# Kernel optimization log

Measured on AMD Instinct MI355X. Metric: run time of the kernel, lower is better.

The kernel has to match this reference:

```python
import jax, jax.numpy as jnp
import numpy as np

E = 8          # moe_num_experts
F = 4096       # ffn_hidden_size
D = 2048       # d_model
TOP_K = 2


def setup_inputs() -> dict:
    key = jax.random.key(0)
    k_x, k_r, k_w1, k_v1, k_w2 = jax.random.split(key, 5)
    scale = 0.02  # ~ normal initializer scale
    x = jax.random.normal(k_x, (2, 2048, D), dtype=jnp.float32)
    router_w = jax.random.normal(k_r, (D, E), dtype=jnp.float32) * scale
    w1 = jax.random.normal(k_w1, (E * F, D), dtype=jnp.float32) * scale
    v1 = jax.random.normal(k_v1, (E * F, D), dtype=jnp.float32) * scale
    w2 = jax.random.normal(k_w2, (E * F, D), dtype=jnp.float32) * scale
    return {"x": x, "router_w": router_w, "w1": w1, "v1": v1, "w2": w2}


def reference(x, router_w, w1, v1, w2):
    # --- Router: dense logits -> softmax (fp32) -> top-k -> L1 normalize ---
    logits = jnp.einsum("bsd,de->bse", x.astype(jnp.float32), router_w)
    weights = jax.nn.softmax(logits, axis=-1)                       # [B,S,E]
    top_weights, top_experts = jax.lax.top_k(weights, TOP_K)        # [B,S,K]
    # moe_normalize_expert_weights = 1 -> L1 norm
    top_weights = top_weights / jnp.sum(jnp.abs(top_weights), axis=-1, keepdims=True)
    top_weights = top_weights.astype(x.dtype)

    # --- Experts: dense per-expert GLU, masked combine (faithful to source) ---
    w1r = w1.reshape(E, F, D)
    v1r = v1.reshape(E, F, D)
    w2r = w2.reshape(E, F, D)
    out = jnp.zeros_like(x)
    for e in range(E):  # fixed small structural loop over experts
        x1 = jnp.einsum("bsd,fd->bsf", x, w1r[e])
        x2 = jnp.einsum("bsd,fd->bsf", x, v1r[e])
        h = jax.nn.silu(x1) * x2                                    # GLU
        y = jnp.einsum("bsf,fd->bsd", h, w2r[e])
        coef = jnp.sum((top_experts == e) * top_weights, axis=-1)[:, :, None]
        out = out + coef * y
    return out
```

## Files before the change

### kernel.cpp

```cpp
#include <hip/hip_runtime.h>
#include <cstdio>
#include <cstdint>

typedef _Float16 f16;
typedef _Float16 f16x8 __attribute__((ext_vector_type(8)));
typedef float f32x4 __attribute__((ext_vector_type(4)));

#define D_MODEL 2048
#define FFN     4096
#define FFN2    8192
#define NEXP    8
#define NTOK    4096
#define NENT    (NTOK*2)
#define BM      256
#define BN      256
#define BK      64
#define MAX_ROWS  10240
#define MAX_TILES 40

__device__ __forceinline__ void gload_lds16(const void* g, void* l) {
  __builtin_amdgcn_global_load_lds(
      (const __attribute__((address_space(1))) void*)g,
      (__attribute__((address_space(3))) void*)l, 16, 0, 0);
}

template<int N> __device__ __forceinline__ void waitvm() {
  if constexpr (N == 0) asm volatile("s_waitcnt vmcnt(0)" ::: "memory");
  else if constexpr (N == 2) asm volatile("s_waitcnt vmcnt(2)" ::: "memory");
  else if constexpr (N == 4) asm volatile("s_waitcnt vmcnt(4)" ::: "memory");
  else if constexpr (N == 6) asm volatile("s_waitcnt vmcnt(6)" ::: "memory");
}

template<int LD>
__device__ __forceinline__ void stageA(const f16* aT, int k0, f16* AS, int mh, int tid) {
#pragma unroll
  for (int s = 0; s < 2; s++) {
    int o = s*8192 + tid*16;
    int rl = o >> 7;
    int ce = ((o & 127) ^ ((rl & 7) << 4)) >> 1;
    int arow = s*128 + mh*64 + (rl & 63);
    gload_lds16(aT + (size_t)arow * LD + k0 + ce,
                (char*)AS + mh*16384 + s*8192 + (tid & ~63)*16);
  }
}

template<int LD>
__device__ __forceinline__ void stageB(const f16* bT, int k0, f16* BS, int nh, int tid) {
#pragma unroll
  for (int s = 0; s < 2; s++) {
    int o = s*8192 + tid*16;
    int rl = o >> 7;
    int ce = ((o & 127) ^ ((rl & 7) << 4)) >> 1;
    int crow = (rl >> 5)*64 + nh*32 + (rl & 31);
    gload_lds16(bT + (size_t)crow * LD + k0 + ce,
                (char*)BS + nh*16384 + s*8192 + (tid & ~63)*16);
  }
}

__device__ __forceinline__ f16x8 fragLd(const f16* S, int row, int lane, int ks) {
  int kb = ks*64 + (lane >> 4)*16;
  int off = (row*128 + kb) ^ ((row & 7) << 4);
  return *(const f16x8*)((const char*)S + off);
}

template<int LD, int V0, int V1, int V3, bool SB0, bool SB1, bool SA1, bool SA0>
__device__ __forceinline__ void tile4(
    const f16* aT, const f16* bT, int k1, int k2,
    f16* ASc, f16* BSc, f16* ASn, f16* BSn,
    f32x4 (&acc)[8][4], f16x8 (&aF)[4][2], f16x8 (&bF)[2][2][2],
    int tid, int lane, int wrM, int wcN) {
#pragma unroll
  for (int mf = 0; mf < 4; mf++)
#pragma unroll
    for (int ks = 0; ks < 2; ks++)
      aF[mf][ks] = fragLd(ASc, wrM*64 + mf*16 + (lane & 15), lane, ks);
#pragma unroll
  for (int nf = 0; nf < 2; nf++)
#pragma unroll
    for (int ks = 0; ks < 2; ks++)
      bF[0][nf][ks] = fragLd(BSc, wcN*32 + nf*16 + (lane & 15), lane, ks);
  if constexpr (SB0) stageB<LD>(bT, k1, BSn, 0, tid);
  __builtin_amdgcn_s_barrier();
  __builtin_amdgcn_s_setprio(1);
#pragma unroll
  for (int mf = 0; mf < 4; mf++)
#pragma unroll
    for (int nf = 0; nf < 2; nf++)
#pragma unroll
      for (int ks = 0; ks < 2; ks++)
        acc[mf][nf] = __builtin_amdgcn_mfma_f32_16x16x32_f16(aF[mf][ks], bF[0][nf][ks], acc[mf][nf], 0, 0, 0);
  __builtin_amdgcn_s_setprio(0);
  waitvm<V0>();
  __builtin_amdgcn_s_barrier();
#pragma unroll
  for (int nf = 0; nf < 2; nf++)
#pragma unroll
    for (int ks = 0; ks < 2; ks++)
      bF[1][nf][ks] = fragLd(BSc, 128 + wcN*32 + nf*16 + (lane & 15), lane, ks);
  if constexpr (SB1) stageB<LD>(bT, k1, BSn, 1, tid);
  __builtin_amdgcn_s_barrier();
  __builtin_amdgcn_s_setprio(1);
#pragma unroll
  for (int mf = 0; mf < 4; mf++)
#pragma unroll
    for (int nf = 0; nf < 2; nf++)
#pragma unroll
      for (int ks = 0; ks < 2; ks++)
        acc[mf][2+nf] = __builtin_amdgcn_mfma_f32_16x16x32_f16(aF[mf][ks], bF[1][nf][ks], acc[mf][2+nf], 0, 0, 0);
  __builtin_amdgcn_s_setprio(0);
  waitvm<V1>();
  __builtin_amdgcn_s_barrier();
#pragma unroll
  for (int mf = 0; mf < 4; mf++)
#pragma unroll
    for (int ks = 0; ks < 2; ks++)
      aF[mf][ks] = fragLd(ASc, 128 + wrM*64 + mf*16 + (lane & 15), lane, ks);
  if constexpr (SA1) stageA<LD>(aT, k1, ASn, 1, tid);
  __builtin_amdgcn_s_barrier();
  __builtin_amdgcn_s_setprio(1);
#pragma unroll
  for (int mf = 0; mf < 4; mf++)
#pragma unroll
    for (int nf = 0; nf < 2; nf++)
#pragma unroll
      for (int ks = 0; ks < 2; ks++)
        acc[4+mf][nf] = __builtin_amdgcn_mfma_f32_16x16x32_f16(aF[mf][ks], bF[0][nf][ks], acc[4+mf][nf], 0, 0, 0);
  __builtin_amdgcn_s_setprio(0);
  __builtin_amdgcn_s_barrier();
  if constexpr (SA0) stageA<LD>(aT, k2, ASc, 0, tid);
  __builtin_amdgcn_s_barrier();
  __builtin_amdgcn_s_setprio(1);
#pragma unroll
  for (int mf = 0; mf < 4; mf++)
#pragma unroll
    for (int nf = 0; nf < 2; nf++)
#pragma unroll
      for (int ks = 0; ks < 2; ks++)
        acc[4+mf][2+nf] = __builtin_amdgcn_mfma_f32_16x16x32_f16(aF[mf][ks], bF[1][nf][ks], acc[4+mf][2+nf], 0, 0, 0);
  __builtin_amdgcn_s_setprio(0);
  waitvm<V3>();
  __builtin_amdgcn_s_barrier();
}


__global__ void zero_counts_kernel(int* counts) {
  if (threadIdx.x < NEXP) counts[threadIdx.x] = 0;
}

__global__ void zero_f32_kernel(float* p, int n4) {
  int i = blockIdx.x * blockDim.x + threadIdx.x;
  int stride = gridDim.x * blockDim.x;
  float4 z = {0.f, 0.f, 0.f, 0.f};
  for (; i < n4; i += stride) ((float4*)p)[i] = z;
}

__global__ __launch_bounds__(64) void router_kernel(
    const float* __restrict__ x, const float* __restrict__ rw,
    int* counts, int* te, float* tw, int* trank) {
  int t = blockIdx.x;
  int lane = threadIdx.x;
  float acc[8] = {0.f,0.f,0.f,0.f,0.f,0.f,0.f,0.f};
  const float* xr = x + (size_t)t * D_MODEL;
  for (int d = lane; d < D_MODEL; d += 64) {
    float xv = xr[d];
    const float4* r4 = (const float4*)(rw + (size_t)d * NEXP);
    float4 a = r4[0], b = r4[1];
    acc[0] += xv*a.x; acc[1] += xv*a.y; acc[2] += xv*a.z; acc[3] += xv*a.w;
    acc[4] += xv*b.x; acc[5] += xv*b.y; acc[6] += xv*b.z; acc[7] += xv*b.w;
  }
#pragma unroll
  for (int off = 32; off > 0; off >>= 1) {
#pragma unroll
    for (int e = 0; e < 8; e++) acc[e] += __shfl_down(acc[e], off);
  }
  if (lane == 0) {
    int e0 = 0;
#pragma unroll
    for (int e = 1; e < 8; e++) if (acc[e] > acc[e0]) e0 = e;
    int e1 = (e0 == 0) ? 1 : 0;
#pragma unroll
    for (int e = 0; e < 8; e++) if (e != e0 && acc[e] > acc[e1]) e1 = e;
    float c0 = 1.0f / (1.0f + expf(acc[e1] - acc[e0]));
    float c1 = 1.0f - c0;
    int r0 = atomicAdd(&counts[e0], 1);
    int r1 = atomicAdd(&counts[e1], 1);
    te[t*2] = e0; te[t*2+1] = e1;
    tw[t*2] = c0; tw[t*2+1] = c1;
    trank[t*2] = r0; trank[t*2+1] = r1;
  }
}

__global__ void sched_kernel(const int* counts, int* offsets, int4* sched, int* nT) {
  if (threadIdx.x != 0 || blockIdx.x != 0) return;
  int off = 0, n = 0;
  for (int e = 0; e < NEXP; e++) {
    offsets[e] = off;
    int cnt = counts[e];
    int nt = (cnt + BM - 1) / BM;
    for (int i = 0; i < nt; i++) {
      sched[n] = make_int4(e, off + i*BM, min(BM, cnt - i*BM), 0);
      n++;
    }
    off += nt * BM;
  }
  offsets[NEXP] = off;
  *nT = n;
}

__global__ __launch_bounds__(256) void gather_kernel(
    const float* __restrict__ x, const int* __restrict__ te,
    const float* __restrict__ tw, const int* __restrict__ trank,
    const int* __restrict__ offsets, f16* __restrict__ xg,
    int* __restrict__ token_of, float* __restrict__ coefs) {
  int i = blockIdx.x;
  int t = i >> 1;
  int e = te[i];
  int slot = offsets[e] + trank[i];
  if (threadIdx.x == 0) { token_of[slot] = t; coefs[slot] = tw[i]; }
  const float4* src = (const float4*)(x + (size_t)t * D_MODEL);
  f16x8* dst = (f16x8*)(xg + (size_t)slot * D_MODEL);
  for (int j = threadIdx.x; j < D_MODEL/8; j += 256) {
    float4 v0 = src[j*2], v1 = src[j*2+1];
    f16x8 h;
    h[0]=(f16)v0.x; h[1]=(f16)v0.y; h[2]=(f16)v0.z; h[3]=(f16)v0.w;
    h[4]=(f16)v1.x; h[5]=(f16)v1.y; h[6]=(f16)v1.z; h[7]=(f16)v1.w;
    dst[j] = h;
  }
}

__global__ __launch_bounds__(256) void convert_ileave_kernel(
    const float* __restrict__ src, f16* __restrict__ dst, int parity) {
  int n8 = NEXP*FFN*D_MODEL/8;
  int stride = gridDim.x * 256;
  for (int i = blockIdx.x*256 + threadIdx.x; i < n8; i += stride) {
    int d8 = i & (D_MODEL/8 - 1);
    int fr_glob = i >> 8;
    int e = fr_glob >> 12;
    int fr = fr_glob & (FFN - 1);
    int cr = ((fr >> 4)*2 + parity)*16 + (fr & 15);
    float4 v0 = ((const float4*)src)[(size_t)i*2];
    float4 v1 = ((const float4*)src)[(size_t)i*2 + 1];
    f16x8 h;
    h[0]=(f16)v0.x; h[1]=(f16)v0.y; h[2]=(f16)v0.z; h[3]=(f16)v0.w;
    h[4]=(f16)v1.x; h[5]=(f16)v1.y; h[6]=(f16)v1.z; h[7]=(f16)v1.w;
    ((f16x8*)dst)[((size_t)e*FFN2 + cr)*(D_MODEL/8) + d8] = h;
  }
}

__global__ __launch_bounds__(256) void transpose_w2_kernel(
    const float* __restrict__ w2, f16* __restrict__ w2t) {
  __shared__ float tl[64][65];
  int e = blockIdx.z;
  int d0 = blockIdx.x * 64, f0 = blockIdx.y * 64;
  const float* src = w2 + (size_t)e * FFN * D_MODEL;
  int tid = threadIdx.x;
  int fr = tid >> 4, c4 = (tid & 15) * 4;
#pragma unroll
  for (int rr = 0; rr < 4; rr++) {
    float4 v = *(const float4*)(src + (size_t)(f0 + fr + rr*16) * D_MODEL + d0 + c4);
    tl[fr + rr*16][c4+0] = v.x; tl[fr + rr*16][c4+1] = v.y;
    tl[fr + rr*16][c4+2] = v.z; tl[fr + rr*16][c4+3] = v.w;
  }
  __syncthreads();
  int dr = tid >> 2, fg = (tid & 3) * 16;
  f16* dst = w2t + (size_t)e * D_MODEL * FFN + (size_t)(d0 + dr) * FFN + f0 + fg;
  f16 tmp[16];
#pragma unroll
  for (int j = 0; j < 16; j++) tmp[j] = (f16)tl[fg + j][dr];
  *(float4*)(dst)     = *(float4*)(tmp);
  *(float4*)(dst + 8) = *(float4*)(tmp + 8);
}

__global__ __launch_bounds__(512, 2) void phaseA_kernel(
    const f16* __restrict__ xg, const f16* __restrict__ w12h,
    f16* __restrict__ hbuf, const int4* __restrict__ sched, const int* __restrict__ nT) {
  int tile = blockIdx.y;
  if (tile >= *nT) return;
  int4 sc = sched[tile];
  int e = sc.x, row0 = sc.y;
  int fc0 = blockIdx.x * BN;

  __shared__ f16 AS[2][BM*BK];
  __shared__ f16 BS[2][BN*BK];

  int tid = threadIdx.x, lane = tid & 63, wid = tid >> 6;
  int wrM = wid >> 2, wcN = wid & 3;

  const f16* aT = xg  + (size_t)row0 * D_MODEL;
  const f16* bT = w12h + (size_t)e * FFN2 * D_MODEL + (size_t)fc0 * D_MODEL;

  f32x4 acc[8][4]; f16x8 aF[4][2]; f16x8 bF[2][2][2];
  f32x4 z4 = {0.f,0.f,0.f,0.f};
#pragma unroll
  for (int m = 0; m < 8; m++)
#pragma unroll
    for (int n = 0; n < 4; n++) acc[m][n] = z4;

  stageA<D_MODEL>(aT, 0, AS[0], 0, tid);
  stageB<D_MODEL>(bT, 0, BS[0], 0, tid);
  stageB<D_MODEL>(bT, 0, BS[0], 1, tid);
  stageA<D_MODEL>(aT, 0, AS[0], 1, tid);
  stageA<D_MODEL>(aT, BK, AS[1], 0, tid);
  waitvm<6>();
  __builtin_amdgcn_s_barrier();

  constexpr int NTILES = D_MODEL / BK;
  for (int t = 0; t + 2 < NTILES; t++) {
    int b = t & 1;
    tile4<D_MODEL,6,6,6,true,true,true,true>(aT, bT, (t+1)*BK, (t+2)*BK,
        AS[b], BS[b], AS[b^1], BS[b^1], acc, aF, bF, tid, lane, wrM, wcN);
  }
  { int b = (NTILES-2) & 1;
    tile4<D_MODEL,6,6,4,true,true,true,false>(aT, bT, (NTILES-1)*BK, 0,
        AS[b], BS[b], AS[b^1], BS[b^1], acc, aF, bF, tid, lane, wrM, wcN); }
  { int b = (NTILES-1) & 1;
    tile4<D_MODEL,2,0,-1,false,false,false,false>(aT, bT, 0, 0,
        AS[b], BS[b], AS[b^1], BS[b^1], acc, aF, bF, tid, lane, wrM, wcN); }

  int i15 = lane & 15, l4 = lane >> 4;
#pragma unroll
  for (int m = 0; m < 8; m++) {
    int rowl = wrM*128 + (m>>2)*64 + (m&3)*16 + l4*4;
#pragma unroll
    for (int nh = 0; nh < 2; nh++) {
      int f = (fc0 >> 1) + wcN*32 + nh*16 + i15;
      f16* hb = hbuf + (size_t)(row0 + rowl) * FFN + f;
#pragma unroll
      for (int q = 0; q < 4; q++) {
        float x1 = acc[m][nh*2+0][q], x2 = acc[m][nh*2+1][q];
        float hv = x1 / (1.0f + __expf(-x1)) * x2;
        hb[(size_t)q * FFN] = (f16)hv;
      }
    }
  }
}

__global__ __launch_bounds__(512, 2) void phaseB_kernel(
    const f16* __restrict__ hbuf, const f16* __restrict__ w2t,
    float* __restrict__ out, const int4* __restrict__ sched, const int* __restrict__ nT,
    const int* __restrict__ token_of, const float* __restrict__ coefs) {
  int tile = blockIdx.y;
  if (tile >= *nT) return;
  int4 sc = sched[tile];
  int e = sc.x, row0 = sc.y, valid = sc.z;
  int dc0 = blockIdx.x * BN;

  __shared__ f16 AS[2][BM*BK];
  __shared__ f16 BS[2][BN*BK];

  int tid = threadIdx.x, lane = tid & 63, wid = tid >> 6;
  int wrM = wid >> 2, wcN = wid & 3;

  const f16* aT = hbuf + (size_t)row0 * FFN;
  const f16* bT = w2t + (size_t)e * D_MODEL * FFN + (size_t)dc0 * FFN;

  f32x4 acc[8][4]; f16x8 aF[4][2]; f16x8 bF[2][2][2];
  f32x4 z4 = {0.f,0.f,0.f,0.f};
#pragma unroll
  for (int m = 0; m < 8; m++)
#pragma unroll
    for (int n = 0; n < 4; n++) acc[m][n] = z4;

  stageA<FFN>(aT, 0, AS[0], 0, tid);
  stageB<FFN>(bT, 0, BS[0], 0, tid);
  stageB<FFN>(bT, 0, BS[0], 1, tid);
  stageA<FFN>(aT, 0, AS[0], 1, tid);
  stageA<FFN>(aT, BK, AS[1], 0, tid);
  waitvm<6>();
  __builtin_amdgcn_s_barrier();

  constexpr int NTILES = FFN / BK;
  for (int t = 0; t + 2 < NTILES; t++) {
    int b = t & 1;
    tile4<FFN,6,6,6,true,true,true,true>(aT, bT, (t+1)*BK, (t+2)*BK,
        AS[b], BS[b], AS[b^1], BS[b^1], acc, aF, bF, tid, lane, wrM, wcN);
  }
  { int b = (NTILES-2) & 1;
    tile4<FFN,6,6,4,true,true,true,false>(aT, bT, (NTILES-1)*BK, 0,
        AS[b], BS[b], AS[b^1], BS[b^1], acc, aF, bF, tid, lane, wrM, wcN); }
  { int b = (NTILES-1) & 1;
    tile4<FFN,2,0,-1,false,false,false,false>(aT, bT, 0, 0,
        AS[b], BS[b], AS[b^1], BS[b^1], acc, aF, bF, tid, lane, wrM, wcN); }

  int i15 = lane & 15, l4 = lane >> 4;
#pragma unroll
  for (int m = 0; m < 8; m++) {
#pragma unroll
    for (int q = 0; q < 4; q++) {
      int rl = wrM*128 + (m>>2)*64 + (m&3)*16 + l4*4 + q;
      if (rl < valid) {
        int slot = row0 + rl;
        int t = token_of[slot];
        float cf = coefs[slot];
        float* orow = out + (size_t)t * D_MODEL + dc0 + wcN*64;
#pragma unroll
        for (int n = 0; n < 4; n++)
          atomicAdd(orow + (n>>1)*32 + (n&1)*16 + i15, cf * acc[m][n][q]);
      }
    }
  }
}

extern "C" void kernel_launch(void* const* d_in, const int* in_sizes, int n_in,
                              void* d_out, int out_size, void* d_ws, size_t ws_size,
                              hipStream_t stream) {
  const float* x  = (const float*)d_in[0];
  const float* rw = (const float*)d_in[1];
  const float* w1 = (const float*)d_in[2];
  const float* v1 = (const float*)d_in[3];
  const float* w2 = (const float*)d_in[4];
  float* out = (float*)d_out;

  char* p = (char*)d_ws;
  auto alloc = [&](size_t bytes) {
    char* r = p;
    p += (bytes + 255) & ~(size_t)255;
    return r;
  };
  int*   counts   = (int*)  alloc(NEXP * 4);
  int*   nT       = (int*)  alloc(4);
  int*   offsets  = (int*)  alloc((NEXP + 1) * 4);
  int*   te       = (int*)  alloc(NENT * 4);
  float* tw       = (float*)alloc(NENT * 4);
  int*   trank    = (int*)  alloc(NENT * 4);
  int*   token_of = (int*)  alloc(MAX_ROWS * 4);
  float* coefs    = (float*)alloc(MAX_ROWS * 4);
  int4*  sched    = (int4*) alloc(MAX_TILES * 16);
  f16*   xg       = (f16*)  alloc((size_t)MAX_ROWS * D_MODEL * 2);
  f16*   hbuf     = (f16*)  alloc((size_t)MAX_ROWS * FFN * 2);
  f16*   w12h     = (f16*)  alloc((size_t)NEXP * FFN2 * D_MODEL * 2);
  f16*   w2t      = (f16*)  alloc((size_t)NEXP * FFN * D_MODEL * 2);
  size_t needed = (size_t)(p - (char*)d_ws);
  if (needed > ws_size) {
    fprintf(stderr, "kernel_launch: ws too small: need %zu, have %zu\n", needed, ws_size);
    return;
  }

  zero_counts_kernel<<<1, 64, 0, stream>>>(counts);
  zero_f32_kernel<<<2048, 256, 0, stream>>>(out, out_size / 4);
  router_kernel<<<NTOK, 64, 0, stream>>>(x, rw, counts, te, tw, trank);
  sched_kernel<<<1, 1, 0, stream>>>(counts, offsets, sched, nT);
  gather_kernel<<<NENT, 256, 0, stream>>>(x, te, tw, trank, offsets, xg, token_of, coefs);
  convert_ileave_kernel<<<4096, 256, 0, stream>>>(w1, w12h, 0);
  convert_ileave_kernel<<<4096, 256, 0, stream>>>(v1, w12h, 1);
  transpose_w2_kernel<<<dim3(D_MODEL/64, FFN/64, NEXP), 256, 0, stream>>>(w2, w2t);
  phaseA_kernel<<<dim3(FFN2/BN, MAX_TILES), 512, 0, stream>>>(xg, w12h, hbuf, sched, nT);
  phaseB_kernel<<<dim3(D_MODEL/BN, MAX_TILES), 512, 0, stream>>>(hbuf, w2t, out, sched, nT, token_of, coefs);
}
```

Measured before the change: 945.0 us.

## Split-K the down-projection GEMM and replace atomics with a gather combine kernel

The second expert GEMM is split four ways along the FFN dimension, which raises the block count so more CUs are busy. Each split writes fp16 partial results into reused workspace buffers (xg and w12h) instead of doing fp32 atomicAdd scatter into the output. A new combine kernel gathers each token's two expert slots across all splits, applies the routing weights and writes the output once, so the separate output-zeroing kernel is removed. The cost is extra partial-result traffic, fp16 rounding of the partial sums, and reliance on the reused buffers being large enough and no longer needed.

After: 897.8 us. 1.05x faster.

```diff
diff --git a/kernel.cpp b/kernel.cpp
--- a/kernel.cpp
+++ b/kernel.cpp
@@ -15,6 +15,8 @@
 #define BM      256
 #define BN      256
 #define BK      64
+#define KSPLIT  4
+#define KCHUNK  (FFN / KSPLIT)
 #define MAX_ROWS  10240
 #define MAX_TILES 40
 
@@ -145,13 +147,6 @@
 
 __global__ void zero_counts_kernel(int* counts) {
   if (threadIdx.x < NEXP) counts[threadIdx.x] = 0;
-}
-
-__global__ void zero_f32_kernel(float* p, int n4) {
-  int i = blockIdx.x * blockDim.x + threadIdx.x;
-  int stride = gridDim.x * blockDim.x;
-  float4 z = {0.f, 0.f, 0.f, 0.f};
-  for (; i < n4; i += stride) ((float4*)p)[i] = z;
 }
 
 __global__ __launch_bounds__(64) void router_kernel(
@@ -337,13 +332,14 @@
 
 __global__ __launch_bounds__(512, 2) void phaseB_kernel(
     const f16* __restrict__ hbuf, const f16* __restrict__ w2t,
-    float* __restrict__ out, const int4* __restrict__ sched, const int* __restrict__ nT,
-    const int* __restrict__ token_of, const float* __restrict__ coefs) {
+    f16* __restrict__ yb0, f16* __restrict__ ybR,
+    const int4* __restrict__ sched, const int* __restrict__ nT) {
   int tile = blockIdx.y;
   if (tile >= *nT) return;
   int4 sc = sched[tile];
-  int e = sc.x, row0 = sc.y, valid = sc.z;
+  int e = sc.x, row0 = sc.y;
   int dc0 = blockIdx.x * BN;
+  int z = blockIdx.z;
 
   __shared__ f16 AS[2][BM*BK];
   __shared__ f16 BS[2][BN*BK];
@@ -351,8 +347,8 @@
   int tid = threadIdx.x, lane = tid & 63, wid = tid >> 6;
   int wrM = wid >> 2, wcN = wid & 3;
 
-  const f16* aT = hbuf + (size_t)row0 * FFN;
-  const f16* bT = w2t + (size_t)e * D_MODEL * FFN + (size_t)dc0 * FFN;
+  const f16* aT = hbuf + (size_t)row0 * FFN + z * KCHUNK;
+  const f16* bT = w2t + (size_t)e * D_MODEL * FFN + (size_t)dc0 * FFN + z * KCHUNK;
 
   f32x4 acc[8][4]; f16x8 aF[4][2]; f16x8 bF[2][2][2];
   f32x4 z4 = {0.f,0.f,0.f,0.f};
@@ -369,7 +365,7 @@
   waitvm<6>();
   __builtin_amdgcn_s_barrier();
 
-  constexpr int NTILES = FFN / BK;
+  constexpr int NTILES = KCHUNK / BK;
   for (int t = 0; t + 2 < NTILES; t++) {
     int b = t & 1;
     tile4<FFN,6,6,6,true,true,true,true>(aT, bT, (t+1)*BK, (t+2)*BK,
@@ -382,23 +378,45 @@
     tile4<FFN,2,0,-1,false,false,false,false>(aT, bT, 0, 0,
         AS[b], BS[b], AS[b^1], BS[b^1], acc, aF, bF, tid, lane, wrM, wcN); }
 
+  f16* yb = (z == 0) ? yb0 : (ybR + (size_t)(z-1) * MAX_ROWS * D_MODEL);
   int i15 = lane & 15, l4 = lane >> 4;
 #pragma unroll
   for (int m = 0; m < 8; m++) {
 #pragma unroll
     for (int q = 0; q < 4; q++) {
       int rl = wrM*128 + (m>>2)*64 + (m&3)*16 + l4*4 + q;
-      if (rl < valid) {
-        int slot = row0 + rl;
-        int t = token_of[slot];
-        float cf = coefs[slot];
-        float* orow = out + (size_t)t * D_MODEL + dc0 + wcN*64;
-#pragma unroll
-        for (int n = 0; n < 4; n++)
-          atomicAdd(orow + (n>>1)*32 + (n&1)*16 + i15, cf * acc[m][n][q]);
-      }
+      f16* yrow = yb + (size_t)(row0 + rl) * D_MODEL + dc0 + wcN*64;
+#pragma unroll
+      for (int n = 0; n < 4; n++)
+        yrow[(n>>1)*32 + (n&1)*16 + i15] = (f16)acc[m][n][q];
     }
   }
+}
+
+__global__ __launch_bounds__(256) void combine_kernel(
+    const f16* __restrict__ yb0, const f16* __restrict__ ybR,
+    const int* __restrict__ te, const float* __restrict__ tw,
+    const int* __restrict__ trank, const int* __restrict__ offsets,
+    float* __restrict__ out) {
+  int t = blockIdx.x;
+  int d8 = threadIdx.x;
+  int s0 = offsets[te[2*t]]   + trank[2*t];
+  int s1 = offsets[te[2*t+1]] + trank[2*t+1];
+  float w0 = tw[2*t], w1 = tw[2*t+1];
+  float sum[8] = {0.f,0.f,0.f,0.f,0.f,0.f,0.f,0.f};
+#pragma unroll
+  for (int z = 0; z < KSPLIT; z++) {
+    const f16* yb = (z == 0) ? yb0 : (ybR + (size_t)(z-1) * MAX_ROWS * D_MODEL);
+    f16x8 a = ((const f16x8*)(yb + (size_t)s0 * D_MODEL))[d8];
+    f16x8 b = ((const f16x8*)(yb + (size_t)s1 * D_MODEL))[d8];
+#pragma unroll
+    for (int j = 0; j < 8; j++) sum[j] += w0 * (float)a[j] + w1 * (float)b[j];
+  }
+  float* o = out + (size_t)t * D_MODEL + d8*8;
+  float4 o0 = {sum[0], sum[1], sum[2], sum[3]};
+  float4 o1 = {sum[4], sum[5], sum[6], sum[7]};
+  ((float4*)o)[0] = o0;
+  ((float4*)o)[1] = o1;
 }
 
 extern "C" void kernel_launch(void* const* d_in, const int* in_sizes, int n_in,
@@ -435,9 +453,10 @@
     fprintf(stderr, "kernel_launch: ws too small: need %zu, have %zu\n", needed, ws_size);
     return;
   }
+  f16* yb0 = xg;
+  f16* ybR = w12h;
 
   zero_counts_kernel<<<1, 64, 0, stream>>>(counts);
-  zero_f32_kernel<<<2048, 256, 0, stream>>>(out, out_size / 4);
   router_kernel<<<NTOK, 64, 0, stream>>>(x, rw, counts, te, tw, trank);
   sched_kernel<<<1, 1, 0, stream>>>(counts, offsets, sched, nT);
   gather_kernel<<<NENT, 256, 0, stream>>>(x, te, tw, trank, offsets, xg, token_of, coefs);
@@ -445,5 +464,6 @@
   convert_ileave_kernel<<<4096, 256, 0, stream>>>(v1, w12h, 1);
   transpose_w2_kernel<<<dim3(D_MODEL/64, FFN/64, NEXP), 256, 0, stream>>>(w2, w2t);
   phaseA_kernel<<<dim3(FFN2/BN, MAX_TILES), 512, 0, stream>>>(xg, w12h, hbuf, sched, nT);
-  phaseB_kernel<<<dim3(D_MODEL/BN, MAX_TILES), 512, 0, stream>>>(hbuf, w2t, out, sched, nT, token_of, coefs);
-}
+  phaseB_kernel<<<dim3(D_MODEL/BN, MAX_TILES, KSPLIT), 512, 0, stream>>>(hbuf, w2t, yb0, ybR, sched, nT);
+  combine_kernel<<<NTOK, 256, 0, stream>>>(yb0, ybR, te, tw, trank, offsets, out);
+}
```
